# Kernel optimization log

Measured on AMD Instinct MI355X. Metric: run time of the kernel, lower is better.

Reference implementation:

```python
import jax, jax.numpy as jnp
from jax import lax
import numpy as np

N_HEAD = 16
KERNEL = 3
ROPE_BASE = 10000.0


def _rope_tables(T, D, dtype):
    inv_freq = 1.0 / (ROPE_BASE ** (jnp.arange(0, D, 2, dtype=jnp.float32) / D))
    t = jnp.arange(T, dtype=jnp.float32)
    freqs = t[:, None] * inv_freq[None, :]           # [T, D/2]
    emb = jnp.concatenate([freqs, freqs], axis=-1)   # [T, D]
    return jnp.cos(emb).astype(dtype), jnp.sin(emb).astype(dtype)


def _rotate_half(x):
    x1, x2 = jnp.split(x, 2, axis=-1)
    return jnp.concatenate([-x2, x1], axis=-1)


def setup_inputs() -> dict:
    key = jax.random.key(0)
    k1, k2, k3, k4 = jax.random.split(key, 4)
    B, T, C = 2, 2048, 2048
    s = 0.02
    return {
        "x": jax.random.normal(k1, (B, T, C), dtype=jnp.float32),
        "conv_w": jax.random.normal(k2, (C, 1, KERNEL), dtype=jnp.float32) * s,
        "w_attn": jax.random.normal(k3, (3 * C, C), dtype=jnp.float32) * s,
        "w_proj": jax.random.normal(k4, (C, C), dtype=jnp.float32) * s,
    }


def reference(x, conv_w, w_attn, w_proj):
    B, T, C = x.shape
    H = N_HEAD
    D = C // H

    # causal depthwise conv1d: left-pad K-1, groups=C
    xc = jnp.transpose(x, (0, 2, 1))                       # [B, C, T]
    xc = jnp.pad(xc, ((0, 0), (0, 0), (KERNEL - 1, 0)))
    xc = lax.conv_general_dilated(
        xc, conv_w, window_strides=(1,), padding="VALID",
        feature_group_count=C, dimension_numbers=("NCH", "OIH", "NCH"))
    xconv = jnp.transpose(xc, (0, 2, 1))                   # [B, T, C]

    # fused QKV projection
    qkv = xconv @ w_attn.T                                 # [B, T, 3C]
    q, k, v = jnp.split(qkv, 3, axis=-1)
    q = q.reshape(B, T, H, D)
    k = k.reshape(B, T, H, D)
    v = v.reshape(B, T, H, D)

    # rotary embedding
    cos, sin = _rope_tables(T, D, x.dtype)                 # [T, D]
    cos = cos[None, :, None, :]
    sin = sin[None, :, None, :]
    q = q * cos + _rotate_half(q) * sin
    k = k * cos + _rotate_half(k) * sin

    # causal SDPA
    scale = 1.0 / jnp.sqrt(jnp.asarray(D, dtype=x.dtype))
    scores = jnp.einsum("bthd,bshd->bhts", q, k) * scale   # [B, H, T, T]
    causal = jnp.tril(jnp.ones((T, T), dtype=bool))
    scores = jnp.where(causal[None, None], scores, jnp.finfo(scores.dtype).min)
    p = jax.nn.softmax(scores, axis=-1)
    y = jnp.einsum("bhts,bshd->bthd", p, v).reshape(B, T, C)

    return y @ w_proj.T
```

## Files before the change

### kernel.cpp

```cpp
#include <hip/hip_runtime.h>

typedef __attribute__((ext_vector_type(8))) short bf16x8;
typedef __attribute__((ext_vector_type(4))) float f32x4;
typedef __attribute__((ext_vector_type(4))) unsigned short u16x4;

#define DEV static __device__ __forceinline__

DEV float bf2f(unsigned short u) {
  union { unsigned int i; float f; } v; v.i = ((unsigned int)u) << 16; return v.f;
}
DEV unsigned short f2bf(float f) {
  unsigned int x = __float_as_uint(f);
  x += 0x7fffu + ((x >> 16) & 1u);
  return (unsigned short)(x >> 16);
}
DEV f32x4 mfma16(bf16x8 a, bf16x8 b, f32x4 c) {
  return __builtin_amdgcn_mfma_f32_16x16x32_bf16(a, b, c, 0, 0, 0);
}
DEV void gload_lds16(const void* g, void* l) {
  __builtin_amdgcn_global_load_lds(
      (const __attribute__((address_space(1))) unsigned int*)g,
      (__attribute__((address_space(3))) unsigned int*)l, 16, 0, 0);
}

__global__ void build_tables(float* __restrict__ ct, float* __restrict__ st) {
  int idx = blockIdx.x * 256 + threadIdx.x;
  int i = idx & 63, t = idx >> 6;
  float f = powf(10000.0f, -(float)i * (1.0f / 64.0f));
  float a = (float)t * f;
  ct[idx] = cosf(a);
  st[idx] = sinf(a);
}

__global__ void cast_bf(const float* __restrict__ in, unsigned short* __restrict__ out, int n4) {
  int idx = blockIdx.x * 256 + threadIdx.x;
  if (idx >= n4) return;
  f32x4 v = *(const f32x4*)(in + (size_t)idx * 4);
  u16x4 o;
  #pragma unroll
  for (int j = 0; j < 4; ++j) o[j] = f2bf(v[j]);
  *(u16x4*)(out + (size_t)idx * 4) = o;
}

__global__ void conv_cast(const float* __restrict__ x, const float* __restrict__ w,
                          unsigned short* __restrict__ out) {
  int idx = blockIdx.x * 256 + threadIdx.x;
  int c4 = idx & 511, t = (idx >> 9) & 2047;
  int c = c4 * 4;
  const float* xp = x + (size_t)(idx >> 20) * 2048 * 2048 + (size_t)t * 2048 + c;
  f32x4 v2 = *(const f32x4*)xp;
  f32x4 v1 = {0.f, 0.f, 0.f, 0.f}, v0 = {0.f, 0.f, 0.f, 0.f};
  if (t >= 1) v1 = *(const f32x4*)(xp - 2048);
  if (t >= 2) v0 = *(const f32x4*)(xp - 4096);
  u16x4 o;
  #pragma unroll
  for (int j = 0; j < 4; ++j) {
    float val = v0[j] * w[(c + j) * 3 + 0] + v1[j] * w[(c + j) * 3 + 1] + v2[j] * w[(c + j) * 3 + 2];
    o[j] = f2bf(val);
  }
  *(u16x4*)(out + (size_t)idx * 4) = o;
}

template <bool OUT_BF16>
__global__ __launch_bounds__(256) void gemm_bt(const unsigned short* __restrict__ A,
                                               const unsigned short* __restrict__ Bw,
                                               void* __restrict__ Cp, int M, int N, int K) {
  __shared__ __align__(16) unsigned short As[128 * 32];
  __shared__ __align__(16) unsigned short Bs[128 * 32];
  const int tid = threadIdx.x;
  const int w = tid >> 6, l = tid & 63;
  const int lr = l & 15, lg = l >> 4;
  const int m0 = blockIdx.y * 128, n0 = blockIdx.x * 128;
  const int wr = w >> 1, wc = w & 1;
  f32x4 acc[4][4] = {};
  for (int k0 = 0; k0 < K; k0 += 32) {
    #pragma unroll
    for (int q = 0; q < 2; ++q) {
      int c = q * 256 + tid;
      gload_lds16(A + (size_t)(m0 + (c >> 2)) * K + k0 + (c & 3) * 8, As + (q * 256 + w * 64) * 8);
      gload_lds16(Bw + (size_t)(n0 + (c >> 2)) * K + k0 + (c & 3) * 8, Bs + (q * 256 + w * 64) * 8);
    }
    __syncthreads();
    bf16x8 af[4], bf[4];
    #pragma unroll
    for (int m = 0; m < 4; ++m) af[m] = *(const bf16x8*)(As + (wr * 64 + m * 16 + lr) * 32 + lg * 8);
    #pragma unroll
    for (int n = 0; n < 4; ++n) bf[n] = *(const bf16x8*)(Bs + (wc * 64 + n * 16 + lr) * 32 + lg * 8);
    #pragma unroll
    for (int m = 0; m < 4; ++m)
      #pragma unroll
      for (int n = 0; n < 4; ++n) acc[m][n] = mfma16(af[m], bf[n], acc[m][n]);
    __syncthreads();
  }
  #pragma unroll
  for (int m = 0; m < 4; ++m)
    #pragma unroll
    for (int r = 0; r < 4; ++r) {
      int row = m0 + wr * 64 + m * 16 + lg * 4 + r;
      #pragma unroll
      for (int n = 0; n < 4; ++n) {
        int col = n0 + wc * 64 + n * 16 + lr;
        if (OUT_BF16) ((unsigned short*)Cp)[(size_t)row * N + col] = f2bf(acc[m][n][r]);
        else          ((float*)Cp)[(size_t)row * N + col] = acc[m][n][r];
      }
    }
}

__global__ void rope_repack(const unsigned short* __restrict__ qkv, const float* __restrict__ ct,
                            const float* __restrict__ st, unsigned short* __restrict__ Qo,
                            unsigned short* __restrict__ Ko) {
  int idx = blockIdx.x * 256 + threadIdx.x;
  int i = idx & 63;
  int h = (idx >> 6) & 15;
  int t = (idx >> 10) & 2047;
  int b = idx >> 21;
  const unsigned short* src = qkv + ((size_t)(b * 2048 + t)) * 6144 + h * 128;
  float cz = ct[t * 64 + i], sz = st[t * 64 + i];
  float q1 = bf2f(src[i]),        q2 = bf2f(src[i + 64]);
  float k1 = bf2f(src[2048 + i]), k2 = bf2f(src[2048 + i + 64]);
  size_t o = ((size_t)(b * 16 + h) * 2048 + t) * 128 + i;
  Qo[o]      = f2bf(q1 * cz - q2 * sz);
  Qo[o + 64] = f2bf(q2 * cz + q1 * sz);
  Ko[o]      = f2bf(k1 * cz - k2 * sz);
  Ko[o + 64] = f2bf(k2 * cz + k1 * sz);
}

__global__ __launch_bounds__(256) void v_transpose(const unsigned short* __restrict__ qkv,
                                                   unsigned short* __restrict__ Vt) {
  __shared__ unsigned short tile[64][72];
  const int bh = blockIdx.x;
  const int tt = blockIdx.y;
  const int dd = blockIdx.z;
  const int b = bh >> 4, h = bh & 15;
  const unsigned short* src = qkv + ((size_t)(b * 2048 + tt * 64)) * 6144 + 4096 + h * 128 + dd * 64;
  const int row = threadIdx.x >> 2;
  const int ch = threadIdx.x & 3;
  #pragma unroll
  for (int it = 0; it < 2; ++it) {
    int d0 = (ch * 2 + it) * 8;
    *(bf16x8*)&tile[row][d0] = *(const bf16x8*)(src + (size_t)row * 6144 + d0);
  }
  __syncthreads();
  unsigned short* dst = Vt + ((size_t)bh * 128 + dd * 64) * 2048 + tt * 64;
  #pragma unroll
  for (int it = 0; it < 2; ++it) {
    int t0 = (ch * 2 + it) * 8;
    bf16x8 v;
    #pragma unroll
    for (int j = 0; j < 8; ++j) ((unsigned short*)&v)[j] = tile[t0 + j][row];
    *(bf16x8*)(dst + (size_t)row * 2048 + t0) = v;
  }
}

__global__ __launch_bounds__(256, 4) void attn_fwd(const unsigned short* __restrict__ Q,
                                                   const unsigned short* __restrict__ K,
                                                   const unsigned short* __restrict__ Vt,
                                                   unsigned short* __restrict__ Y) {
  const int T = 2048, D = 128, C = 2048;
  __shared__ __align__(16) unsigned short Ks[64 * 128];
  __shared__ __align__(16) unsigned short Vs[128 * 64];
  __shared__ __align__(16) unsigned short Pl[4][16 * 64];
  const int tid = threadIdx.x;
  const int w = tid >> 6, l = tid & 63;
  const int lr = l & 15, lg = l >> 4;
  const int bh = blockIdx.x;
  const int qi = (int)gridDim.y - 1 - (int)blockIdx.y;
  const int qbase = qi * 64;
  const size_t base = (size_t)bh * T * D;

  bf16x8 qf[4];
  {
    const unsigned short* qp = Q + base + (size_t)(qbase + w * 16 + lr) * D + lg * 8;
    #pragma unroll
    for (int d = 0; d < 4; ++d) qf[d] = *(const bf16x8*)(qp + d * 32);
  }
  int kSrc[4], vSrc[4], ldsDst[4];
  #pragma unroll
  for (int it = 0; it < 4; ++it) {
    int c = it * 256 + tid;
    int krow = c >> 4, kdc = c & 15;
    kSrc[it] = krow * D + ((kdc ^ (krow & 7)) * 8);
    int vd = c >> 3, vcc = c & 7;
    vSrc[it] = vd * T + ((vcc ^ (vd & 7)) * 8);
    ldsDst[it] = (it * 256 + w * 64) * 8;
  }
  f32x4 ao[8] = {};
  float mrun = -3.0e38f, lrun = 0.0f;
  const float cs = 0.08838834764831845f * 1.4426950408889634f;
  const int q_abs = qbase + w * 16 + lr;

  for (int kt = 0; kt <= qi; ++kt) {
    const int kv0 = kt * 64;
    #pragma unroll
    for (int it = 0; it < 4; ++it) {
      gload_lds16(K + base + (size_t)kv0 * D + kSrc[it], Ks + ldsDst[it]);
      gload_lds16(Vt + base + kv0 + vSrc[it], Vs + ldsDst[it]);
    }
    __syncthreads();
    f32x4 s4[4] = {};
    __builtin_amdgcn_s_setprio(1);
    #pragma unroll
    for (int n = 0; n < 4; ++n) {
      int row = n * 16 + lr;
      #pragma unroll
      for (int d = 0; d < 4; ++d) {
        bf16x8 kf = *(const bf16x8*)(Ks + row * 128 + (((d * 4 + lg) ^ (lr & 7)) * 8));
        s4[n] = mfma16(kf, qf[d], s4[n]);
      }
    }
    __builtin_amdgcn_s_setprio(0);
    if (kt == qi) {
      #pragma unroll
      for (int n = 0; n < 4; ++n)
        #pragma unroll
        for (int r = 0; r < 4; ++r)
          if (kv0 + n * 16 + lg * 4 + r > q_abs) s4[n][r] = -3.0e38f;
    }
    float mx = -3.0e38f;
    #pragma unroll
    for (int n = 0; n < 4; ++n)
      #pragma unroll
      for (int r = 0; r < 4; ++r) mx = fmaxf(mx, s4[n][r]);
    mx = fmaxf(mx, __shfl_xor(mx, 16, 64));
    mx = fmaxf(mx, __shfl_xor(mx, 32, 64));
    float mnew = fmaxf(mrun, mx);
    float fac = exp2f((mrun - mnew) * cs);
    mrun = mnew;
    float sum = 0.0f;
    #pragma unroll
    for (int n = 0; n < 4; ++n)
      #pragma unroll
      for (int r = 0; r < 4; ++r) {
        float p = exp2f((s4[n][r] - mnew) * cs);
        s4[n][r] = p;
        sum += p;
      }
    sum += __shfl_xor(sum, 16, 64);
    sum += __shfl_xor(sum, 32, 64);
    lrun = lrun * fac + sum;
    float fr[4];
    #pragma unroll
    for (int r = 0; r < 4; ++r) fr[r] = __shfl(fac, (l & 48) | (lg * 4 + r), 64);
    #pragma unroll
    for (int n8 = 0; n8 < 8; ++n8)
      #pragma unroll
      for (int r = 0; r < 4; ++r) ao[n8][r] *= fr[r];
    unsigned short* pw = (unsigned short*)Pl[w];
    #pragma unroll
    for (int n = 0; n < 4; ++n)
      #pragma unroll
      for (int i = 0; i < 2; ++i) {
        unsigned int pk = (unsigned int)f2bf(s4[n][2 * i]) |
                          ((unsigned int)f2bf(s4[n][2 * i + 1]) << 16);
        int kv = n * 16 + lg * 4 + 2 * i;
        *(unsigned int*)(pw + lr * 64 + (((kv >> 3) ^ (lr & 7)) * 8) + (kv & 7)) = pk;
      }
    __builtin_amdgcn_s_setprio(1);
    #pragma unroll
    for (int ks = 0; ks < 2; ++ks) {
      bf16x8 pa = *(const bf16x8*)(pw + lr * 64 + (((ks * 4 + lg) ^ (lr & 7)) * 8));
      #pragma unroll
      for (int n = 0; n < 8; ++n) {
        int row = n * 16 + lr;
        bf16x8 vb = *(const bf16x8*)(Vs + row * 64 + (((ks * 4 + lg) ^ (lr & 7)) * 8));
        ao[n] = mfma16(pa, vb, ao[n]);
      }
    }
    __builtin_amdgcn_s_setprio(0);
    __syncthreads();
  }
  const int b = bh >> 4, h = bh & 15;
  #pragma unroll
  for (int r = 0; r < 4; ++r) {
    float lsum = __shfl(lrun, (l & 48) | (lg * 4 + r), 64);
    float inv = 1.0f / lsum;
    int t = qbase + w * 16 + lg * 4 + r;
    unsigned short* dst = Y + ((size_t)b * T + t) * C + h * D;
    #pragma unroll
    for (int n = 0; n < 8; ++n) dst[n * 16 + lr] = f2bf(ao[n][r] * inv);
  }
}

extern "C" void kernel_launch(void* const* d_in, const int* in_sizes, int n_in,
                              void* d_out, int out_size, void* d_ws, size_t ws_size,
                              hipStream_t stream) {
  const float* x      = (const float*)d_in[0];
  const float* conv_w = (const float*)d_in[1];
  const float* w_attn = (const float*)d_in[2];
  const float* w_proj = (const float*)d_in[3];
  float* out = (float*)d_out;
  char* ws = (char*)d_ws;

  unsigned short* qkv  = (unsigned short*)(ws);
  unsigned short* qb   = (unsigned short*)(ws + 50331648);
  unsigned short* kb   = (unsigned short*)(ws + 67108864);
  unsigned short* vt   = (unsigned short*)(ws + 83886080);
  unsigned short* xcy  = (unsigned short*)(ws + 100663296);
  unsigned short* wbuf = (unsigned short*)(ws + 117440512);
  float* ctab = (float*)(ws + 142606336);
  float* stab = (float*)(ws + 143130624);

  build_tables<<<512, 256, 0, stream>>>(ctab, stab);
  cast_bf<<<12288, 256, 0, stream>>>(w_attn, wbuf, 3145728);
  conv_cast<<<8192, 256, 0, stream>>>(x, conv_w, xcy);
  gemm_bt<true><<<dim3(48, 32), 256, 0, stream>>>(xcy, wbuf, (void*)qkv, 4096, 6144, 2048);
  rope_repack<<<16384, 256, 0, stream>>>(qkv, ctab, stab, qb, kb);
  v_transpose<<<dim3(32, 32, 2), 256, 0, stream>>>(qkv, vt);
  cast_bf<<<4096, 256, 0, stream>>>(w_proj, wbuf, 1048576);
  attn_fwd<<<dim3(32, 32), 256, 0, stream>>>(qb, kb, vt, xcy);
  gemm_bt<false><<<dim3(16, 32), 256, 0, stream>>>(xcy, wbuf, (void*)out, 4096, 2048, 2048);
}
```

Baseline: 327.4 us.

## Rewrite bf16 GEMM with 256x256 tiles, double-buffered swizzled LDS and XCD block remap

Replaces the 128x128x32 single-buffered GEMM with a 512-thread kernel that computes 256x256 output tiles with a K-step of 64. It prefetches the next K tile into a second LDS buffer via direct global-to-LDS loads while the current tile feeds MFMA. The LDS layout uses an XOR swizzle to avoid bank conflicts, and block ids are remapped across XCDs for better L2 locality. Both the QKV and output projections switch to it; the output projection now launches only 128 blocks, which may leave CUs idle, and the large LDS footprint limits occupancy.

```diff
diff --git a/kernel.cpp b/kernel.cpp
--- a/kernel.cpp
+++ b/kernel.cpp
@@ -62,44 +62,93 @@
 }
 
 template <bool OUT_BF16>
-__global__ __launch_bounds__(256) void gemm_bt(const unsigned short* __restrict__ A,
-                                               const unsigned short* __restrict__ Bw,
-                                               void* __restrict__ Cp, int M, int N, int K) {
-  __shared__ __align__(16) unsigned short As[128 * 32];
-  __shared__ __align__(16) unsigned short Bs[128 * 32];
+__global__ __launch_bounds__(512, 2) void gemm_bt2(const unsigned short* __restrict__ A,
+                                                   const unsigned short* __restrict__ Bw,
+                                                   void* __restrict__ Cp, int M, int N, int K) {
+  __shared__ __align__(16) unsigned short As[2][256 * 64];
+  __shared__ __align__(16) unsigned short Bs[2][256 * 64];
   const int tid = threadIdx.x;
   const int w = tid >> 6, l = tid & 63;
   const int lr = l & 15, lg = l >> 4;
-  const int m0 = blockIdx.y * 128, n0 = blockIdx.x * 128;
-  const int wr = w >> 1, wc = w & 1;
-  f32x4 acc[4][4] = {};
-  for (int k0 = 0; k0 < K; k0 += 32) {
-    #pragma unroll
-    for (int q = 0; q < 2; ++q) {
-      int c = q * 256 + tid;
-      gload_lds16(A + (size_t)(m0 + (c >> 2)) * K + k0 + (c & 3) * 8, As + (q * 256 + w * 64) * 8);
-      gload_lds16(Bw + (size_t)(n0 + (c >> 2)) * K + k0 + (c & 3) * 8, Bs + (q * 256 + w * 64) * 8);
-    }
-    __syncthreads();
-    bf16x8 af[4], bf[4];
-    #pragma unroll
-    for (int m = 0; m < 4; ++m) af[m] = *(const bf16x8*)(As + (wr * 64 + m * 16 + lr) * 32 + lg * 8);
-    #pragma unroll
-    for (int n = 0; n < 4; ++n) bf[n] = *(const bf16x8*)(Bs + (wc * 64 + n * 16 + lr) * 32 + lg * 8);
-    #pragma unroll
-    for (int m = 0; m < 4; ++m)
-      #pragma unroll
-      for (int n = 0; n < 4; ++n) acc[m][n] = mfma16(af[m], bf[n], acc[m][n]);
-    __syncthreads();
-  }
-  #pragma unroll
-  for (int m = 0; m < 4; ++m)
+  const int wm = w >> 2, wn = w & 3;
+  const int nbx = N >> 8, nby = M >> 8;
+  const int nwg = nbx * nby;
+  const int bid = blockIdx.x;
+  const int wg = (bid & 7) * (nwg >> 3) + (bid >> 3);
+  const int bx = wg / nby, by = wg % nby;
+  const int m0 = by << 8, n0 = bx << 8;
+
+  int aSrc[4], bSrc[4], dstOff[4];
+  #pragma unroll
+  for (int it = 0; it < 4; ++it) {
+    int c = it * 512 + tid;
+    int r = c >> 3, cc = (c & 7) ^ (r & 7);
+    aSrc[it] = (m0 + r) * K + cc * 8;
+    bSrc[it] = (n0 + r) * K + cc * 8;
+    dstOff[it] = (it * 512 + w * 64) * 8;
+  }
+  int aRow[8], bRow[4], swz[2];
+  #pragma unroll
+  for (int m = 0; m < 8; ++m) aRow[m] = (wm * 128 + m * 16 + lr) * 64;
+  #pragma unroll
+  for (int n = 0; n < 4; ++n) bRow[n] = (wn * 64 + n * 16 + lr) * 64;
+  swz[0] = ((0 + lg) ^ (lr & 7)) * 8;
+  swz[1] = ((4 + lg) ^ (lr & 7)) * 8;
+
+  f32x4 acc[8][4] = {};
+  const int NT = K >> 6;
+  #pragma unroll
+  for (int it = 0; it < 4; ++it) {
+    gload_lds16(A + (size_t)aSrc[it], (unsigned short*)As[0] + dstOff[it]);
+    gload_lds16(Bw + (size_t)bSrc[it], (unsigned short*)Bs[0] + dstOff[it]);
+  }
+  __builtin_amdgcn_sched_barrier(0);
+
+  for (int t = 0; t < NT; ++t) {
+    const int cur = t & 1;
+    if (t + 1 < NT) {
+      const int k1 = (t + 1) << 6;
+      #pragma unroll
+      for (int it = 0; it < 4; ++it) {
+        gload_lds16(A + (size_t)(aSrc[it] + k1), (unsigned short*)As[cur ^ 1] + dstOff[it]);
+        gload_lds16(Bw + (size_t)(bSrc[it] + k1), (unsigned short*)Bs[cur ^ 1] + dstOff[it]);
+      }
+      __builtin_amdgcn_sched_barrier(0);
+      asm volatile("s_waitcnt vmcnt(8)" ::: "memory");
+    } else {
+      __builtin_amdgcn_sched_barrier(0);
+      asm volatile("s_waitcnt vmcnt(0)" ::: "memory");
+    }
+    __builtin_amdgcn_s_barrier();
+    __builtin_amdgcn_sched_barrier(0);
+    const unsigned short* Ab = As[cur];
+    const unsigned short* Bb = Bs[cur];
+    #pragma unroll
+    for (int ks = 0; ks < 2; ++ks) {
+      bf16x8 aF[8], bF[4];
+      #pragma unroll
+      for (int m = 0; m < 8; ++m) aF[m] = *(const bf16x8*)(Ab + aRow[m] + swz[ks]);
+      #pragma unroll
+      for (int n = 0; n < 4; ++n) bF[n] = *(const bf16x8*)(Bb + bRow[n] + swz[ks]);
+      __builtin_amdgcn_s_setprio(1);
+      #pragma unroll
+      for (int m = 0; m < 8; ++m)
+        #pragma unroll
+        for (int n = 0; n < 4; ++n) acc[m][n] = mfma16(aF[m], bF[n], acc[m][n]);
+      __builtin_amdgcn_s_setprio(0);
+    }
+    __builtin_amdgcn_sched_barrier(0);
+    __builtin_amdgcn_s_barrier();
+    __builtin_amdgcn_sched_barrier(0);
+  }
+  #pragma unroll
+  for (int m = 0; m < 8; ++m)
     #pragma unroll
     for (int r = 0; r < 4; ++r) {
-      int row = m0 + wr * 64 + m * 16 + lg * 4 + r;
+      int row = m0 + wm * 128 + m * 16 + lg * 4 + r;
       #pragma unroll
       for (int n = 0; n < 4; ++n) {
-        int col = n0 + wc * 64 + n * 16 + lr;
+        int col = n0 + wn * 64 + n * 16 + lr;
         if (OUT_BF16) ((unsigned short*)Cp)[(size_t)row * N + col] = f2bf(acc[m][n][r]);
         else          ((float*)Cp)[(size_t)row * N + col] = acc[m][n][r];
       }
@@ -303,10 +352,10 @@
   build_tables<<<512, 256, 0, stream>>>(ctab, stab);
   cast_bf<<<12288, 256, 0, stream>>>(w_attn, wbuf, 3145728);
   conv_cast<<<8192, 256, 0, stream>>>(x, conv_w, xcy);
-  gemm_bt<true><<<dim3(48, 32), 256, 0, stream>>>(xcy, wbuf, (void*)qkv, 4096, 6144, 2048);
+  gemm_bt2<true><<<384, 512, 0, stream>>>(xcy, wbuf, (void*)qkv, 4096, 6144, 2048);
   rope_repack<<<16384, 256, 0, stream>>>(qkv, ctab, stab, qb, kb);
   v_transpose<<<dim3(32, 32, 2), 256, 0, stream>>>(qkv, vt);
   cast_bf<<<4096, 256, 0, stream>>>(w_proj, wbuf, 1048576);
   attn_fwd<<<dim3(32, 32), 256, 0, stream>>>(qb, kb, vt, xcy);
-  gemm_bt<false><<<dim3(16, 32), 256, 0, stream>>>(xcy, wbuf, (void*)out, 4096, 2048, 2048);
-}
+  gemm_bt2<false><<<128, 512, 0, stream>>>(xcy, wbuf, (void*)out, 4096, 2048, 2048);
+}
```

Result: slower. 335.5 us (+2.5%).

## Replace GEMM with 256-row tiled, double-buffered, swizzled 8-wave kernel

Applied to the files above, without the earlier changes.

Replaces the simple 128x128 single-buffered bf16 GEMM with an 8-wave, 256xBN tile kernel. It stages K=64 chunks through double-buffered LDS with async global-to-LDS loads issued one to two steps ahead, XOR-swizzled LDS layout, explicit vmcnt waits and priority bumps around MFMA bursts. It also remaps block IDs for better L2 locality. The goal is to hide global load latency and reduce LDS bank conflicts and barrier stalls in both projection GEMMs. The cost is more LDS use, more register pressure from larger accumulators, and fragile hand-tuned waitcnt sequencing.

```diff
diff --git a/kernel.cpp b/kernel.cpp
--- a/kernel.cpp
+++ b/kernel.cpp
@@ -58,48 +58,121 @@
     float val = v0[j] * w[(c + j) * 3 + 0] + v1[j] * w[(c + j) * 3 + 1] + v2[j] * w[(c + j) * 3 + 2];
     o[j] = f2bf(val);
   }
-  *(u16x4*)(out + (size_t)idx * 4) = o;
-}
-
-template <bool OUT_BF16>
-__global__ __launch_bounds__(256) void gemm_bt(const unsigned short* __restrict__ A,
-                                               const unsigned short* __restrict__ Bw,
-                                               void* __restrict__ Cp, int M, int N, int K) {
-  __shared__ __align__(16) unsigned short As[128 * 32];
-  __shared__ __align__(16) unsigned short Bs[128 * 32];
+  *(u16x4*)(idx * 4 + out) = o;
+}
+
+template <int NFRAG, bool OUT_BF16>
+__global__ __launch_bounds__(512, 2) void gemm8(const unsigned short* __restrict__ A,
+                                                const unsigned short* __restrict__ Bw,
+                                                void* __restrict__ Cp, int M, int N, int K) {
+  constexpr int BN = NFRAG * 64;
+  constexpr int BLD = (NFRAG >= 4) ? 2 : 1;
+  __shared__ __align__(16) unsigned short As[2][2][256 * 32];
+  __shared__ __align__(16) unsigned short Bs[2][2][BN * 32];
   const int tid = threadIdx.x;
   const int w = tid >> 6, l = tid & 63;
   const int lr = l & 15, lg = l >> 4;
-  const int m0 = blockIdx.y * 128, n0 = blockIdx.x * 128;
-  const int wr = w >> 1, wc = w & 1;
-  f32x4 acc[4][4] = {};
-  for (int k0 = 0; k0 < K; k0 += 32) {
-    #pragma unroll
-    for (int q = 0; q < 2; ++q) {
-      int c = q * 256 + tid;
-      gload_lds16(A + (size_t)(m0 + (c >> 2)) * K + k0 + (c & 3) * 8, As + (q * 256 + w * 64) * 8);
-      gload_lds16(Bw + (size_t)(n0 + (c >> 2)) * K + k0 + (c & 3) * 8, Bs + (q * 256 + w * 64) * 8);
-    }
-    __syncthreads();
-    bf16x8 af[4], bf[4];
-    #pragma unroll
-    for (int m = 0; m < 4; ++m) af[m] = *(const bf16x8*)(As + (wr * 64 + m * 16 + lr) * 32 + lg * 8);
-    #pragma unroll
-    for (int n = 0; n < 4; ++n) bf[n] = *(const bf16x8*)(Bs + (wc * 64 + n * 16 + lr) * 32 + lg * 8);
-    #pragma unroll
-    for (int m = 0; m < 4; ++m)
-      #pragma unroll
-      for (int n = 0; n < 4; ++n) acc[m][n] = mfma16(af[m], bf[n], acc[m][n]);
-    __syncthreads();
-  }
-  #pragma unroll
-  for (int m = 0; m < 4; ++m)
+  const int wm = w >> 2, wn = w & 3;
+  const int nbx = N / BN, nby = M >> 8;
+  const int nwg = nbx * nby;
+  const int bid = blockIdx.x;
+  const int wg = (bid & 7) * (nwg >> 3) + (bid >> 3);
+  const int bx = wg / nby, by = wg % nby;
+  const int m0 = by << 8, n0 = bx * BN;
+
+  int aOff[2], bOff[2];
+  #pragma unroll
+  for (int it = 0; it < 2; ++it) {
+    int q = it * 512 + tid, row = q >> 2, cp = q & 3;
+    aOff[it] = (m0 + row) * K + ((cp ^ ((row >> 1) & 3)) * 8);
+  }
+  #pragma unroll
+  for (int it = 0; it < BLD; ++it) {
+    int q = it * 512 + tid, row = q >> 2, cp = q & 3;
+    bOff[it] = (n0 + row) * K + ((cp ^ ((row >> 1) & 3)) * 8);
+  }
+  const int dstW = w * 64 * 8;
+
+  int aRd[8], bRd[NFRAG];
+  #pragma unroll
+  for (int m = 0; m < 8; ++m) {
+    int R = wm * 128 + m * 16 + lr;
+    aRd[m] = R * 32 + ((lg ^ ((R >> 1) & 3)) * 8);
+  }
+  #pragma unroll
+  for (int n = 0; n < NFRAG; ++n) {
+    int R = wn * (NFRAG * 16) + n * 16 + lr;
+    bRd[n] = R * 32 + ((lg ^ ((R >> 1) & 3)) * 8);
+  }
+
+  auto stageA = [&](int tt, int kh) {
+    const unsigned short* s = A + (size_t)(tt * 64 + kh * 32);
+    unsigned short* d = (unsigned short*)As[tt & 1][kh] + dstW;
+    gload_lds16(s + aOff[0], d);
+    gload_lds16(s + aOff[1], d + 4096);
+  };
+  auto stageB = [&](int tt, int kh) {
+    const unsigned short* s = Bw + (size_t)(tt * 64 + kh * 32);
+    unsigned short* d = (unsigned short*)Bs[tt & 1][kh] + dstW;
+    gload_lds16(s + bOff[0], d);
+    if constexpr (BLD == 2) gload_lds16(s + bOff[1], d + 4096);
+  };
+  #define WAIT_STEADY()                                            \
+    if constexpr (NFRAG == 4) asm volatile("s_waitcnt vmcnt(4)" ::: "memory"); \
+    else                      asm volatile("s_waitcnt vmcnt(3)" ::: "memory")
+
+  f32x4 acc[8][NFRAG] = {};
+  const int NT = K >> 6;
+  stageA(0, 0); stageB(0, 0); stageA(0, 1); stageB(0, 1);
+  stageA(1, 0); stageB(1, 0);
+  __builtin_amdgcn_sched_barrier(0);
+  WAIT_STEADY();
+  __builtin_amdgcn_s_barrier();
+  __builtin_amdgcn_sched_barrier(0);
+
+  #define PHASE(KH, MH, STAGE_STMT, WAIT_STMT)                                  \
+  {                                                                             \
+    const unsigned short* Ab = (const unsigned short*)As[t & 1][KH];            \
+    const unsigned short* Bb = (const unsigned short*)Bs[t & 1][KH];            \
+    bf16x8 aF[4], bF[NFRAG];                                                    \
+    _Pragma("unroll") for (int j = 0; j < 4; ++j)                               \
+        aF[j] = *(const bf16x8*)(Ab + aRd[MH * 4 + j]);                         \
+    _Pragma("unroll") for (int n = 0; n < NFRAG; ++n)                           \
+        bF[n] = *(const bf16x8*)(Bb + bRd[n]);                                  \
+    STAGE_STMT;                                                                 \
+    __builtin_amdgcn_sched_barrier(0);                                          \
+    __builtin_amdgcn_s_barrier();                                               \
+    __builtin_amdgcn_sched_barrier(0);                                          \
+    __builtin_amdgcn_s_setprio(1);                                              \
+    _Pragma("unroll") for (int j = 0; j < 4; ++j)                               \
+      _Pragma("unroll") for (int n = 0; n < NFRAG; ++n)                         \
+          acc[MH * 4 + j][n] = mfma16(aF[j], bF[n], acc[MH * 4 + j][n]);        \
+    __builtin_amdgcn_s_setprio(0);                                              \
+    WAIT_STMT;                                                                  \
+    __builtin_amdgcn_sched_barrier(0);                                          \
+    __builtin_amdgcn_s_barrier();                                               \
+    __builtin_amdgcn_sched_barrier(0);                                          \
+  }
+
+  for (int t = 0; t < NT; ++t) {
+    PHASE(0, 0, { if (t + 1 < NT) stageA(t + 1, 1); }, {});
+    PHASE(0, 1, { if (t + 1 < NT) stageB(t + 1, 1); }, {});
+    PHASE(1, 0, { if (t + 2 < NT) stageA(t + 2, 0); }, {});
+    PHASE(1, 1, { if (t + 2 < NT) stageB(t + 2, 0); },
+          { if (t + 2 < NT) { WAIT_STEADY(); }
+            else asm volatile("s_waitcnt vmcnt(0)" ::: "memory"); });
+  }
+  #undef PHASE
+  #undef WAIT_STEADY
+
+  #pragma unroll
+  for (int m = 0; m < 8; ++m)
     #pragma unroll
     for (int r = 0; r < 4; ++r) {
-      int row = m0 + wr * 64 + m * 16 + lg * 4 + r;
-      #pragma unroll
-      for (int n = 0; n < 4; ++n) {
-        int col = n0 + wc * 64 + n * 16 + lr;
+      int row = m0 + wm * 128 + m * 16 + lg * 4 + r;
+      #pragma unroll
+      for (int n = 0; n < NFRAG; ++n) {
+        int col = n0 + wn * (NFRAG * 16) + n * 16 + lr;
         if (OUT_BF16) ((unsigned short*)Cp)[(size_t)row * N + col] = f2bf(acc[m][n][r]);
         else          ((float*)Cp)[(size_t)row * N + col] = acc[m][n][r];
       }
@@ -303,10 +376,10 @@
   build_tables<<<512, 256, 0, stream>>>(ctab, stab);
   cast_bf<<<12288, 256, 0, stream>>>(w_attn, wbuf, 3145728);
   conv_cast<<<8192, 256, 0, stream>>>(x, conv_w, xcy);
-  gemm_bt<true><<<dim3(48, 32), 256, 0, stream>>>(xcy, wbuf, (void*)qkv, 4096, 6144, 2048);
+  gemm8<4, true><<<384, 512, 0, stream>>>(xcy, wbuf, (void*)qkv, 4096, 6144, 2048);
   rope_repack<<<16384, 256, 0, stream>>>(qkv, ctab, stab, qb, kb);
   v_transpose<<<dim3(32, 32, 2), 256, 0, stream>>>(qkv, vt);
   cast_bf<<<4096, 256, 0, stream>>>(w_proj, wbuf, 1048576);
   attn_fwd<<<dim3(32, 32), 256, 0, stream>>>(qb, kb, vt, xcy);
-  gemm_bt<false><<<dim3(16, 32), 256, 0, stream>>>(xcy, wbuf, (void*)out, 4096, 2048, 2048);
-}
+  gemm8<2, false><<<256, 512, 0, stream>>>(xcy, wbuf, (void*)out, 4096, 2048, 2048);
+}
```

New measurement: 318.6 us. 1.03x faster.

## Add XCD-aware block remap and swizzled LDS layout to bf16 GEMM

Applied to the files above, without the earlier changes.

The GEMM now launches as a 1D grid and remaps block IDs so that consecutive workgroups land on the same XCD and walk M-tiles within a column of N. This is meant to improve L2 reuse of the weight tiles. It also XOR-swizzles the 16-byte chunks on both the global-to-LDS load and the LDS fragment reads, to cut LDS bank conflicts. Address offsets are precomputed outside the K loop. The swizzle has to match exactly on the write and read sides, and the offsets now use 32-bit int math.

```diff
diff --git a/kernel.cpp b/kernel.cpp
--- a/kernel.cpp
+++ b/kernel.cpp
@@ -58,38 +58,63 @@
     float val = v0[j] * w[(c + j) * 3 + 0] + v1[j] * w[(c + j) * 3 + 1] + v2[j] * w[(c + j) * 3 + 2];
     o[j] = f2bf(val);
   }
-  *(u16x4*)(out + (size_t)idx * 4) = o;
+  *(u16x4*)(idx * 4 + out) = o;
 }
 
 template <bool OUT_BF16>
-__global__ __launch_bounds__(256) void gemm_bt(const unsigned short* __restrict__ A,
-                                               const unsigned short* __restrict__ Bw,
-                                               void* __restrict__ Cp, int M, int N, int K) {
+__global__ __launch_bounds__(256) void gemm97(const unsigned short* __restrict__ A,
+                                              const unsigned short* __restrict__ Bw,
+                                              void* __restrict__ Cp, int M, int N, int K) {
   __shared__ __align__(16) unsigned short As[128 * 32];
   __shared__ __align__(16) unsigned short Bs[128 * 32];
   const int tid = threadIdx.x;
   const int w = tid >> 6, l = tid & 63;
   const int lr = l & 15, lg = l >> 4;
-  const int m0 = blockIdx.y * 128, n0 = blockIdx.x * 128;
   const int wr = w >> 1, wc = w & 1;
+  const int nbx = N >> 7, nby = M >> 7;
+  const int nwg = nbx * nby;
+  const int bid = blockIdx.x;
+  const int wg = (bid & 7) * (nwg >> 3) + (bid >> 3);
+  const int bx = wg / nby, by = wg % nby;
+  const int m0 = by << 7, n0 = bx << 7;
+
+  int aSrc[2], bSrc[2];
+  #pragma unroll
+  for (int it = 0; it < 2; ++it) {
+    int c = it * 256 + tid, R = c >> 2, p = c & 3;
+    int g = ((((p >> 1) ^ (R & 1)) << 1) | (p & 1)) * 8;
+    aSrc[it] = (m0 + R) * K + g;
+    bSrc[it] = (n0 + R) * K + g;
+  }
+  int aRd[4], bRd[4];
+  #pragma unroll
+  for (int m = 0; m < 4; ++m) {
+    int R = wr * 64 + m * 16 + lr;
+    aRd[m] = R * 32 + ((((lg >> 1) ^ (R & 1)) << 1) | (lg & 1)) * 8;
+  }
+  #pragma unroll
+  for (int n = 0; n < 4; ++n) {
+    int R = wc * 64 + n * 16 + lr;
+    bRd[n] = R * 32 + ((((lg >> 1) ^ (R & 1)) << 1) | (lg & 1)) * 8;
+  }
+
   f32x4 acc[4][4] = {};
   for (int k0 = 0; k0 < K; k0 += 32) {
     #pragma unroll
-    for (int q = 0; q < 2; ++q) {
-      int c = q * 256 + tid;
-      gload_lds16(A + (size_t)(m0 + (c >> 2)) * K + k0 + (c & 3) * 8, As + (q * 256 + w * 64) * 8);
-      gload_lds16(Bw + (size_t)(n0 + (c >> 2)) * K + k0 + (c & 3) * 8, Bs + (q * 256 + w * 64) * 8);
+    for (int it = 0; it < 2; ++it) {
+      gload_lds16(A + (size_t)(aSrc[it] + k0), As + (it * 256 + w * 64) * 8);
+      gload_lds16(Bw + (size_t)(bSrc[it] + k0), Bs + (it * 256 + w * 64) * 8);
     }
     __syncthreads();
-    bf16x8 af[4], bf[4];
-    #pragma unroll
-    for (int m = 0; m < 4; ++m) af[m] = *(const bf16x8*)(As + (wr * 64 + m * 16 + lr) * 32 + lg * 8);
-    #pragma unroll
-    for (int n = 0; n < 4; ++n) bf[n] = *(const bf16x8*)(Bs + (wc * 64 + n * 16 + lr) * 32 + lg * 8);
+    bf16x8 aF[4], bF[4];
+    #pragma unroll
+    for (int m = 0; m < 4; ++m) aF[m] = *(const bf16x8*)(As + aRd[m]);
+    #pragma unroll
+    for (int n = 0; n < 4; ++n) bF[n] = *(const bf16x8*)(Bs + bRd[n]);
     #pragma unroll
     for (int m = 0; m < 4; ++m)
       #pragma unroll
-      for (int n = 0; n < 4; ++n) acc[m][n] = mfma16(af[m], bf[n], acc[m][n]);
+      for (int n = 0; n < 4; ++n) acc[m][n] = mfma16(aF[m], bF[n], acc[m][n]);
     __syncthreads();
   }
   #pragma unroll
@@ -303,10 +328,10 @@
   build_tables<<<512, 256, 0, stream>>>(ctab, stab);
   cast_bf<<<12288, 256, 0, stream>>>(w_attn, wbuf, 3145728);
   conv_cast<<<8192, 256, 0, stream>>>(x, conv_w, xcy);
-  gemm_bt<true><<<dim3(48, 32), 256, 0, stream>>>(xcy, wbuf, (void*)qkv, 4096, 6144, 2048);
+  gemm97<true><<<1536, 256, 0, stream>>>(xcy, wbuf, (void*)qkv, 4096, 6144, 2048);
   rope_repack<<<16384, 256, 0, stream>>>(qkv, ctab, stab, qb, kb);
   v_transpose<<<dim3(32, 32, 2), 256, 0, stream>>>(qkv, vt);
   cast_bf<<<4096, 256, 0, stream>>>(w_proj, wbuf, 1048576);
   attn_fwd<<<dim3(32, 32), 256, 0, stream>>>(qb, kb, vt, xcy);
-  gemm_bt<false><<<dim3(16, 32), 256, 0, stream>>>(xcy, wbuf, (void*)out, 4096, 2048, 2048);
-}
+  gemm97<false><<<512, 256, 0, stream>>>(xcy, wbuf, (void*)out, 4096, 2048, 2048);
+}
```

Result: no change. 332.5 us (+1.6%).
